# Kernel optimization log

Hardware: AMD Instinct MI355X
Metric: run time of the kernel (lower is better)

The kernel has to match this reference:

```python
import jax, jax.numpy as jnp
import numpy as np

L, D, V, F4 = 12, 768, 50304, 3072
B, T = 4, 1024


def setup_inputs() -> dict:
    key = jax.random.key(0)
    ks = jax.random.split(key, 12)
    s = 0.02
    return {
        "idx": jax.random.randint(ks[0], (B, T), 0, V),
        "targets": jax.random.randint(ks[1], (B, T), 0, V),
        "wte": jax.random.normal(ks[2], (V, D), jnp.float32) * s,  # tied with lm_head
        "pos_embed": jax.random.normal(ks[3], (L, D), jnp.float32),  # per-block (1,1,D) learned pos embed
        "dyt_alpha": jnp.full((L, 3), 0.5, jnp.float32),  # dyt, dyt2, dyt3 alphas
        "dyt_w": jnp.ones((L, 3, D), jnp.float32),
        "dyt_b": jnp.zeros((L, 3, D), jnp.float32),
        "Wq": jax.random.normal(ks[4], (L, D, D), jnp.float32) * s,
        "Wk": jax.random.normal(ks[5], (L, D, D), jnp.float32) * s,
        "Wv": jax.random.normal(ks[6], (L, D, D), jnp.float32) * s,
        "Wp": jax.random.normal(ks[7], (L, D, D), jnp.float32) * s,
        "bp": jnp.zeros((L, D), jnp.float32),
        "We": jax.random.normal(ks[8], (L, F4, D), jnp.float32) * s,
        "be": jnp.zeros((L, F4), jnp.float32),
        "Wc": jax.random.normal(ks[9], (L, D, F4), jnp.float32) * s,
        "bc": jnp.zeros((L, D), jnp.float32),
    }


def _dyt(x, a, w, b):
    return jnp.tanh(a * x) * w + b


def _forward(idx, targets, wte, pos_embed, dyt_alpha, dyt_w, dyt_b,
             Wq, Wk, Wv, Wp, bp, We, be, Wc, bc):
    b, t = idx.shape
    x = wte[idx]  # (b,t,D)
    pos = jnp.arange(t)
    pbias = -jnp.abs(pos[None, :] - pos[:, None]).astype(x.dtype)  # (t,t) ALiBi-style bias
    scale = 1.0 / np.sqrt(D)  # note: source scales by sqrt(emb_dim), not head dim
    total_kl = jnp.asarray(0.0, x.dtype)
    for l in range(L):
        xl = x + pos_embed[l][None, None, :]
        prior = _dyt(xl, dyt_alpha[l, 2], dyt_w[l, 2], dyt_b[l, 2])  # dyt3
        h = _dyt(xl, dyt_alpha[l, 0], dyt_w[l, 0], dyt_b[l, 0])      # dyt (dropout=0)
        Q = jnp.einsum('btd,od->bto', h, Wq[l])
        K = jnp.einsum('btd,od->bto', h, Wk[l])
        Vv = jnp.einsum('btd,od->bto', h, Wv[l])
        scores = jnp.einsum('btd,bsd->bts', Q, K) * scale + pbias  # (b,t,t), no causal mask
        aw = jax.nn.softmax(scores, axis=-1)
        ao = jnp.einsum('bts,bsd->btd', aw, Vv)
        ao = jnp.einsum('btd,od->bto', ao, Wp[l]) + bp[l]
        h2 = _dyt(ao, dyt_alpha[l, 1], dyt_w[l, 1], dyt_b[l, 1])     # dyt2
        h2 = jax.nn.gelu(jnp.einsum('btd,fd->btf', h2, We[l]) + be[l], approximate=False)
        h2 = jnp.einsum('btf,df->btd', h2, Wc[l]) + bc[l]
        posterior = h2 + prior
        m = 0.5 * (prior + posterior)
        lm = jax.nn.log_softmax(m, axis=-1)
        mp = jnp.exp(lm)
        lp = jax.nn.log_softmax(prior, axis=-1)
        lq = jax.nn.log_softmax(posterior, axis=-1)
        # F.kl_div(log_p, q, reduction='batchmean') = sum(q*(log q - log_p)) / batch
        kl = 0.5 * (jnp.sum(mp * (lm - lp)) + jnp.sum(mp * (lm - lq))) / b
        total_kl = total_kl + kl
        x = posterior
    logits = jnp.einsum('btd,vd->btv', x[:, -1:, :], wte)  # (b,1,V)
    full_logits = jnp.einsum('btd,vd->btv', x, wte)
    lsm = jax.nn.log_softmax(full_logits, axis=-1)
    nll = -jnp.take_along_axis(lsm, targets[..., None], axis=-1).squeeze(-1)
    loss = jnp.mean(nll) + total_kl * 0.1
    return logits, loss


def reference(idx, targets, wte, pos_embed, dyt_alpha, dyt_w, dyt_b,
              Wq, Wk, Wv, Wp, bp, We, be, Wc, bc):
    return _forward(idx, targets, wte, pos_embed, dyt_alpha, dyt_w, dyt_b,
                    Wq, Wk, Wv, Wp, bp, We, be, Wc, bc)
```

## Files before the change

kernel.cpp:

```cpp
#include <hip/hip_runtime.h>
#include <hip/hip_bf16.h>

typedef __attribute__((ext_vector_type(8))) short bf16x8;
typedef __attribute__((ext_vector_type(4))) float f32x4;

__device__ __forceinline__ short f2bf(float f) {
  unsigned u = __float_as_uint(f);
  u = u + 0x7fffu + ((u >> 16) & 1u);
  return (short)(u >> 16);
}
__device__ __forceinline__ float bf2f(short s) {
  return __uint_as_float(((unsigned)(unsigned short)s) << 16);
}

#define GLOB_CAST(p) ((const __attribute__((address_space(1))) void*)(p))
#define LDS_CAST(p) ((__attribute__((address_space(3))) void*)(p))
#define GLL16(g, l) __builtin_amdgcn_global_load_lds(GLOB_CAST(g), LDS_CAST(l), 16, 0, 0)

constexpr int EP_BF16 = 0, EP_SCORES = 1, EP_DYT = 2, EP_GELU = 3, EP_PRIOR = 4;

__global__ __launch_bounds__(256) void cvt_k(const float* __restrict__ src,
                                             short* __restrict__ dst, long n4) {
  const long s = (long)blockIdx.x * 256 + threadIdx.x;
  if (s >= n4) return;
  float4 v = ((const float4*)src)[s];
  short4 o = {f2bf(v.x), f2bf(v.y), f2bf(v.z), f2bf(v.w)};
  ((short4*)dst)[s] = o;
}

__global__ __launch_bounds__(256) void cvt_layer_k(
    const float* __restrict__ wq, const float* __restrict__ wk,
    const float* __restrict__ wv, const float* __restrict__ wp,
    const float* __restrict__ we, const float* __restrict__ wc,
    short* __restrict__ dst) {
  const long s = (long)blockIdx.x * 256 + threadIdx.x;
  const long e = s * 4;
  const float* src; long off;
  if (e < 589824)        { src = wq; off = e; }
  else if (e < 1179648)  { src = wk; off = e - 589824; }
  else if (e < 1769472)  { src = wv; off = e - 1179648; }
  else if (e < 2359296)  { src = wp; off = e - 1769472; }
  else if (e < 4718592)  { src = we; off = e - 2359296; }
  else                   { src = wc; off = e - 4718592; }
  float4 v = *(const float4*)(src + off);
  short4 o = {f2bf(v.x), f2bf(v.y), f2bf(v.z), f2bf(v.w)};
  *(short4*)(dst + e) = o;
}

__global__ __launch_bounds__(256) void embed_k(const int* __restrict__ idx,
                                               const float* __restrict__ wte,
                                               float* __restrict__ x) {
  const long s = (long)blockIdx.x * 256 + threadIdx.x;
  const long row = s / 192;
  const int c4 = (int)(s % 192);
  ((float4*)x)[s] = ((const float4*)(wte + (long)idx[row] * 768))[c4];
}

__global__ __launch_bounds__(256) void layerhead_k(
    const float* __restrict__ x, const float* __restrict__ pos,
    const float* __restrict__ alp, const float* __restrict__ w,
    const float* __restrict__ b, float* __restrict__ prior,
    short* __restrict__ h) {
  const long s = (long)blockIdx.x * 256 + threadIdx.x;
  const int c4 = (int)(s % 192);
  float4 xv = ((const float4*)x)[s];
  float4 pv = ((const float4*)pos)[c4];
  float4 w0 = ((const float4*)w)[c4];
  float4 b0 = ((const float4*)b)[c4];
  float4 w2 = ((const float4*)(w + 1536))[c4];
  float4 b2 = ((const float4*)(b + 1536))[c4];
  const float a0 = alp[0], a2 = alp[2];
  float4 xl = {xv.x + pv.x, xv.y + pv.y, xv.z + pv.z, xv.w + pv.w};
  float4 pr = {tanhf(a2 * xl.x) * w2.x + b2.x, tanhf(a2 * xl.y) * w2.y + b2.y,
               tanhf(a2 * xl.z) * w2.z + b2.z, tanhf(a2 * xl.w) * w2.w + b2.w};
  ((float4*)prior)[s] = pr;
  short4 hh = {f2bf(tanhf(a0 * xl.x) * w0.x + b0.x),
               f2bf(tanhf(a0 * xl.y) * w0.y + b0.y),
               f2bf(tanhf(a0 * xl.z) * w0.z + b0.z),
               f2bf(tanhf(a0 * xl.w) * w0.w + b0.w)};
  ((short4*)h)[s] = hh;
}

template <int EP>
__global__ __launch_bounds__(256, 2) void gemm_bt(
    const short* __restrict__ A, const short* __restrict__ B,
    void* __restrict__ Cv, int K, int lda, int ldb, int ldc,
    long sA, long sB, long sC,
    const float* __restrict__ bias, const float* __restrict__ dw,
    const float* __restrict__ db, const float* __restrict__ alp,
    const float* __restrict__ prior, float scale) {
  __shared__ short As[128 * 64];
  __shared__ short Bs[128 * 64];
  const int tid = threadIdx.x, lane = tid & 63;
  const int wr = tid >> 7, wc = (tid >> 6) & 1;
  const long rowBase = (long)blockIdx.y * 128;
  const long colBase = (long)blockIdx.x * 128;
  const short* Ab = A + (long)blockIdx.z * sA;
  const short* Bb = B + (long)blockIdx.z * sB;
  const int srow = tid >> 3, sseg = tid & 7;
  const int ssegS = sseg ^ (srow & 7);

  f32x4 acc[4][4];
#pragma unroll
  for (int m = 0; m < 4; ++m)
#pragma unroll
    for (int n = 0; n < 4; ++n) acc[m][n] = (f32x4){0.f, 0.f, 0.f, 0.f};

  const int q = lane >> 4, cl = lane & 15;
  const int rsw = cl & 7;

  for (int kt = 0; kt < K; kt += 64) {
#pragma unroll
    for (int i = 0; i < 4; ++i) {
      GLL16(Ab + (rowBase + i * 32 + srow) * (long)lda + kt + ssegS * 8,
            As + ((i * 32 + srow) * 64 + sseg * 8));
      GLL16(Bb + (colBase + i * 32 + srow) * (long)ldb + kt + ssegS * 8,
            Bs + ((i * 32 + srow) * 64 + sseg * 8));
    }
    __syncthreads();
#pragma unroll
    for (int kk = 0; kk < 2; ++kk) {
      const int sw = ((kk * 4 + q) ^ rsw) << 3;
      bf16x8 af[4], bfr[4];
#pragma unroll
      for (int m = 0; m < 4; ++m)
        af[m] = *(const bf16x8*)&As[(wr * 64 + m * 16 + cl) * 64 + sw];
#pragma unroll
      for (int n = 0; n < 4; ++n)
        bfr[n] = *(const bf16x8*)&Bs[(wc * 64 + n * 16 + cl) * 64 + sw];
#pragma unroll
      for (int m = 0; m < 4; ++m)
#pragma unroll
        for (int n = 0; n < 4; ++n)
          acc[m][n] = __builtin_amdgcn_mfma_f32_16x16x32_bf16(af[m], bfr[n], acc[m][n], 0, 0, 0);
    }
    __syncthreads();
  }

#pragma unroll
  for (int m = 0; m < 4; ++m) {
#pragma unroll
    for (int n = 0; n < 4; ++n) {
#pragma unroll
      for (int j = 0; j < 4; ++j) {
        long r = rowBase + wr * 64 + m * 16 + q * 4 + j;
        long c = colBase + wc * 64 + n * 16 + cl;
        float v = acc[m][n][j];
        if constexpr (EP == EP_SCORES) {
          float pb = -fabsf((float)(int)(r - c));
          ((float*)Cv)[(long)blockIdx.z * sC + r * ldc + c] = v * scale + pb;
        } else if constexpr (EP == EP_BF16) {
          ((short*)Cv)[(long)blockIdx.z * sC + r * ldc + c] = f2bf(v);
        } else if constexpr (EP == EP_DYT) {
          float xv = v + bias[c];
          ((short*)Cv)[r * (long)ldc + c] = f2bf(tanhf(alp[0] * xv) * dw[c] + db[c]);
        } else if constexpr (EP == EP_GELU) {
          float xv = v + bias[c];
          ((short*)Cv)[r * (long)ldc + c] = f2bf(0.5f * xv * (1.f + erff(xv * 0.70710678118654752f)));
        } else if constexpr (EP == EP_PRIOR) {
          ((float*)Cv)[r * (long)ldc + c] = v + bias[c] + prior[r * (long)ldc + c];
        }
      }
    }
  }
}

__global__ __launch_bounds__(256) void transp_k(const short* __restrict__ V,
                                                short* __restrict__ Vt, int ldv) {
  __shared__ short t[32][33];
  const int b = blockIdx.z;
  const int d0 = blockIdx.x * 32, t0 = blockIdx.y * 32;
  const int tx = threadIdx.x & 31, ty = threadIdx.x >> 5;
  const short* Vb = V + (long)b * 1024 * ldv;
  short* Tb = Vt + (long)b * 768 * 1024;
#pragma unroll
  for (int i = 0; i < 4; ++i)
    t[ty + i * 8][tx] = Vb[(long)(t0 + ty + i * 8) * ldv + d0 + tx];
  __syncthreads();
#pragma unroll
  for (int i = 0; i < 4; ++i)
    Tb[(long)(d0 + ty + i * 8) * 1024 + t0 + tx] = t[tx][ty + i * 8];
}

__global__ __launch_bounds__(256) void softmax_k(const float* __restrict__ sc,
                                                 short* __restrict__ aw) {
  const int lane = threadIdx.x & 63;
  const long row = (long)blockIdx.x * 4 + (threadIdx.x >> 6);
  const float4* p = (const float4*)(sc + row * 1024);
  float4 v[4];
  float mx = -3e38f;
#pragma unroll
  for (int i = 0; i < 4; ++i) {
    v[i] = p[lane * 4 + i];
    mx = fmaxf(mx, fmaxf(fmaxf(v[i].x, v[i].y), fmaxf(v[i].z, v[i].w)));
  }
#pragma unroll
  for (int o = 1; o < 64; o <<= 1) mx = fmaxf(mx, __shfl_xor(mx, o));
  float e[16];
  float s = 0.f;
#pragma unroll
  for (int i = 0; i < 4; ++i) {
    e[i * 4 + 0] = __expf(v[i].x - mx);
    e[i * 4 + 1] = __expf(v[i].y - mx);
    e[i * 4 + 2] = __expf(v[i].z - mx);
    e[i * 4 + 3] = __expf(v[i].w - mx);
    s += e[i * 4] + e[i * 4 + 1] + e[i * 4 + 2] + e[i * 4 + 3];
  }
#pragma unroll
  for (int o = 1; o < 64; o <<= 1) s += __shfl_xor(s, o);
  const float inv = 1.f / s;
  short4* dst = (short4*)(aw + row * 1024);
#pragma unroll
  for (int i = 0; i < 4; ++i) {
    short4 o4 = {f2bf(e[i * 4] * inv), f2bf(e[i * 4 + 1] * inv),
                 f2bf(e[i * 4 + 2] * inv), f2bf(e[i * 4 + 3] * inv)};
    dst[lane * 4 + i] = o4;
  }
}

__global__ __launch_bounds__(256) void kl_k(const float* __restrict__ prior,
                                            const float* __restrict__ post,
                                            double* __restrict__ acc) {
  const int lane = threadIdx.x & 63;
  const long row = (long)blockIdx.x * 4 + (threadIdx.x >> 6);
  const float* pp = prior + row * 768;
  const float* qq = post + row * 768;
  float p[12], q[12];
#pragma unroll
  for (int i = 0; i < 12; ++i) { p[i] = pp[lane + i * 64]; q[i] = qq[lane + i * 64]; }
  float mp = -3e38f, mq = -3e38f, mm = -3e38f;
#pragma unroll
  for (int i = 0; i < 12; ++i) {
    float m = 0.5f * (p[i] + q[i]);
    mp = fmaxf(mp, p[i]); mq = fmaxf(mq, q[i]); mm = fmaxf(mm, m);
  }
#pragma unroll
  for (int o = 1; o < 64; o <<= 1) {
    mp = fmaxf(mp, __shfl_xor(mp, o));
    mq = fmaxf(mq, __shfl_xor(mq, o));
    mm = fmaxf(mm, __shfl_xor(mm, o));
  }
  float sp = 0.f, sq = 0.f, sm = 0.f;
#pragma unroll
  for (int i = 0; i < 12; ++i) {
    sp += __expf(p[i] - mp);
    sq += __expf(q[i] - mq);
    sm += __expf(0.5f * (p[i] + q[i]) - mm);
  }
#pragma unroll
  for (int o = 1; o < 64; o <<= 1) {
    sp += __shfl_xor(sp, o); sq += __shfl_xor(sq, o); sm += __shfl_xor(sm, o);
  }
  const float lseP = mp + logf(sp), lseQ = mq + logf(sq), lseM = mm + logf(sm);
  float kl = 0.f;
#pragma unroll
  for (int i = 0; i < 12; ++i) {
    float m = 0.5f * (p[i] + q[i]);
    float lm = m - lseM;
    kl += __expf(lm) * (2.f * lm - (p[i] - lseP) - (q[i] - lseQ));
  }
#pragma unroll
  for (int o = 1; o < 64; o <<= 1) kl += __shfl_xor(kl, o);
  if (lane == 0) atomicAdd(&acc[0], (double)kl);
}

__global__ __launch_bounds__(256, 2) void lse_gemm_k(
    const short* __restrict__ Xb, const short* __restrict__ Wt,
    float* __restrict__ pm, float* __restrict__ ps,
    float* __restrict__ logits_out, int G) {
  __shared__ short As[128 * 64];
  __shared__ short Bs[128 * 64];
  __shared__ float pmx[2][128], psm[2][128], rm[128], rs[128];
  const int tid = threadIdx.x, lane = tid & 63;
  const int wr = tid >> 7, wc = (tid >> 6) & 1;
  const int g = blockIdx.x;
  const long rowBase = (long)blockIdx.y * 128;
  const int srow = tid >> 3, sseg = tid & 7;
  const int ssegS = sseg ^ (srow & 7);
  const int q = lane >> 4, cl = lane & 15;
  const int rsw = cl & 7;
  if (tid < 128) { rm[tid] = -3e38f; rs[tid] = 0.f; }

  for (int tile = g; tile < 393; tile += G) {
    const long colBase = (long)tile * 128;
    f32x4 acc[4][4];
#pragma unroll
    for (int m = 0; m < 4; ++m)
#pragma unroll
      for (int n = 0; n < 4; ++n) acc[m][n] = (f32x4){0.f, 0.f, 0.f, 0.f};

    for (int kt = 0; kt < 768; kt += 64) {
#pragma unroll
      for (int i = 0; i < 4; ++i) {
        GLL16(Xb + (rowBase + i * 32 + srow) * 768L + kt + ssegS * 8,
              As + ((i * 32 + srow) * 64 + sseg * 8));
        GLL16(Wt + (colBase + i * 32 + srow) * 768L + kt + ssegS * 8,
              Bs + ((i * 32 + srow) * 64 + sseg * 8));
      }
      __syncthreads();
#pragma unroll
      for (int kk = 0; kk < 2; ++kk) {
        const int sw = ((kk * 4 + q) ^ rsw) << 3;
        bf16x8 af[4], bfr[4];
#pragma unroll
        for (int m = 0; m < 4; ++m)
          af[m] = *(const bf16x8*)&As[(wr * 64 + m * 16 + cl) * 64 + sw];
#pragma unroll
        for (int n = 0; n < 4; ++n)
          bfr[n] = *(const bf16x8*)&Bs[(wc * 64 + n * 16 + cl) * 64 + sw];
#pragma unroll
        for (int m = 0; m < 4; ++m)
#pragma unroll
          for (int n = 0; n < 4; ++n)
            acc[m][n] = __builtin_amdgcn_mfma_f32_16x16x32_bf16(af[m], bfr[n], acc[m][n], 0, 0, 0);
      }
      __syncthreads();
    }

#pragma unroll
    for (int m = 0; m < 4; ++m)
#pragma unroll
      for (int n = 0; n < 4; ++n)
#pragma unroll
        for (int j = 0; j < 4; ++j) {
          long r = rowBase + wr * 64 + m * 16 + q * 4 + j;
          if ((r & 1023) == 1023) {
            long c = colBase + wc * 64 + n * 16 + cl;
            logits_out[(r >> 10) * 50304 + c] = acc[m][n][j];
          }
        }

#pragma unroll
    for (int m = 0; m < 4; ++m) {
#pragma unroll
      for (int j = 0; j < 4; ++j) {
        float mx = acc[m][0][j];
#pragma unroll
        for (int n = 1; n < 4; ++n) mx = fmaxf(mx, acc[m][n][j]);
#pragma unroll
        for (int o = 1; o < 16; o <<= 1) mx = fmaxf(mx, __shfl_xor(mx, o));
        float sm = 0.f;
#pragma unroll
        for (int n = 0; n < 4; ++n) sm += __expf(acc[m][n][j] - mx);
#pragma unroll
        for (int o = 1; o < 16; o <<= 1) sm += __shfl_xor(sm, o);
        if (cl == 0) {
          int lr = wr * 64 + m * 16 + q * 4 + j;
          pmx[wc][lr] = mx;
          psm[wc][lr] = sm;
        }
      }
    }
    __syncthreads();
    if (tid < 128) {
      float m0 = pmx[0][tid], m1 = pmx[1][tid];
      float m2 = fmaxf(m0, m1);
      float s2 = psm[0][tid] * __expf(m0 - m2) + psm[1][tid] * __expf(m1 - m2);
      float mo = rm[tid], mn = fmaxf(mo, m2);
      rs[tid] = rs[tid] * __expf(mo - mn) + s2 * __expf(m2 - mn);
      rm[tid] = mn;
    }
    __syncthreads();
  }
  if (tid < 128) {
    long row = rowBase + tid;
    pm[row * G + g] = rm[tid];
    ps[row * G + g] = rs[tid];
  }
}

__global__ __launch_bounds__(256) void tlog_k(const short* __restrict__ xbf,
                                              const short* __restrict__ wtebf,
                                              const int* __restrict__ targets,
                                              float* __restrict__ tlog) {
  const int lane = threadIdx.x & 63;
  const long row = (long)blockIdx.x * 4 + (threadIdx.x >> 6);
  const long tgt = targets[row];
  const short* a = xbf + row * 768;
  const short* b = wtebf + tgt * 768;
  float s = 0.f;
#pragma unroll
  for (int i = 0; i < 12; ++i) s += bf2f(a[lane + i * 64]) * bf2f(b[lane + i * 64]);
#pragma unroll
  for (int o = 1; o < 64; o <<= 1) s += __shfl_xor(s, o);
  if (lane == 0) tlog[row] = s;
}

__global__ __launch_bounds__(256) void stage2_k(const float* __restrict__ pm,
                                                const float* __restrict__ ps,
                                                const float* __restrict__ tlog,
                                                double* __restrict__ acc, int G) {
  const long row = (long)blockIdx.x * 256 + threadIdx.x;
  float M = -3e38f;
  for (int gi = 0; gi < G; ++gi) M = fmaxf(M, pm[row * G + gi]);
  float S = 0.f;
  for (int gi = 0; gi < G; ++gi) S += ps[row * G + gi] * __expf(pm[row * G + gi] - M);
  float nll = (M + logf(S)) - tlog[row];
#pragma unroll
  for (int o = 1; o < 64; o <<= 1) nll += __shfl_xor(nll, o);
  if ((threadIdx.x & 63) == 0) atomicAdd(&acc[1], (double)nll);
}

__global__ void finalize_k(const double* __restrict__ acc, float* __restrict__ out) {
  if (threadIdx.x == 0)
    out[201216] = (float)(acc[1] / 4096.0 + 0.1 * 0.5 * acc[0] / 4.0);
}

constexpr size_t OFF_WTEBF = 0;
constexpr size_t OFF_LW    = 77266944;
constexpr size_t OFF_X     = 91422720;
constexpr size_t OFF_PRIOR = 104005632;
constexpr size_t OFF_H     = 116588544;
constexpr size_t OFF_QKV   = 122880000;
constexpr size_t OFF_VT    = 141754368;
constexpr size_t OFF_SC    = 148045824;
constexpr size_t OFF_AW    = 164823040;
constexpr size_t OFF_AO    = 173211648;
constexpr size_t OFF_H2    = 179503104;
constexpr size_t OFF_E     = 185794560;
constexpr size_t OFF_XBF   = 210960384;
constexpr size_t OFF_PM    = 217251840;
constexpr size_t OFF_PS    = 217645056;
constexpr size_t OFF_TLOG  = 218038272;
constexpr size_t OFF_ACC   = 218054656;
constexpr size_t WS_NEED   = 218055680;

extern "C" void kernel_launch(void* const* d_in, const int* in_sizes, int n_in,
                              void* d_out, int out_size, void* d_ws, size_t ws_size,
                              hipStream_t stream) {
  const int* idx = (const int*)d_in[0];
  const int* targets = (const int*)d_in[1];
  const float* wte = (const float*)d_in[2];
  const float* pos = (const float*)d_in[3];
  const float* dalpha = (const float*)d_in[4];
  const float* dytw = (const float*)d_in[5];
  const float* dytb = (const float*)d_in[6];
  const float* Wq = (const float*)d_in[7];
  const float* Wk = (const float*)d_in[8];
  const float* Wv = (const float*)d_in[9];
  const float* Wp = (const float*)d_in[10];
  const float* bp = (const float*)d_in[11];
  const float* We = (const float*)d_in[12];
  const float* be = (const float*)d_in[13];
  const float* Wc = (const float*)d_in[14];
  const float* bc = (const float*)d_in[15];
  float* out = (float*)d_out;

  if (ws_size < WS_NEED) return;
  char* ws = (char*)d_ws;
  short* WTEBF = (short*)(ws + OFF_WTEBF);
  short* LW = (short*)(ws + OFF_LW);
  float* X = (float*)(ws + OFF_X);
  float* PRIOR = (float*)(ws + OFF_PRIOR);
  short* H = (short*)(ws + OFF_H);
  short* QKVB = (short*)(ws + OFF_QKV);
  short* VT = (short*)(ws + OFF_VT);
  float* SC = (float*)(ws + OFF_SC);
  short* AW = (short*)(ws + OFF_AW);
  short* AO = (short*)(ws + OFF_AO);
  short* H2 = (short*)(ws + OFF_H2);
  short* E = (short*)(ws + OFF_E);
  short* XBF = (short*)(ws + OFF_XBF);
  float* PM = (float*)(ws + OFF_PM);
  float* PS = (float*)(ws + OFF_PS);
  float* TLOG = (float*)(ws + OFF_TLOG);
  double* ACC = (double*)(ws + OFF_ACC);

  hipMemsetAsync(ACC, 0, 16, stream);
  cvt_k<<<37728, 256, 0, stream>>>(wte, WTEBF, 9658368);
  embed_k<<<3072, 256, 0, stream>>>(idx, wte, X);

  const float scale = 0.03608439182435161f;

  for (int l = 0; l < 12; ++l) {
    layerhead_k<<<3072, 256, 0, stream>>>(X, pos + l * 768, dalpha + l * 3,
                                          dytw + l * 2304, dytb + l * 2304, PRIOR, H);
    cvt_layer_k<<<6912, 256, 0, stream>>>(Wq + (long)l * 589824, Wk + (long)l * 589824,
                                          Wv + (long)l * 589824, Wp + (long)l * 589824,
                                          We + (long)l * 2359296, Wc + (long)l * 2359296, LW);
    gemm_bt<EP_BF16><<<dim3(18, 32, 1), 256, 0, stream>>>(
        H, LW, QKVB, 768, 768, 768, 2304, 0, 0, 0,
        nullptr, nullptr, nullptr, nullptr, nullptr, 0.f);
    transp_k<<<dim3(24, 32, 4), 256, 0, stream>>>(QKVB + 1536, VT, 2304);
    gemm_bt<EP_SCORES><<<dim3(8, 8, 4), 256, 0, stream>>>(
        QKVB, QKVB + 768, SC, 768, 2304, 2304, 1024,
        2359296, 2359296, 1048576, nullptr, nullptr, nullptr, nullptr, nullptr, scale);
    softmax_k<<<1024, 256, 0, stream>>>(SC, AW);
    gemm_bt<EP_BF16><<<dim3(6, 8, 4), 256, 0, stream>>>(
        AW, VT, AO, 1024, 1024, 1024, 768, 1048576, 786432, 786432,
        nullptr, nullptr, nullptr, nullptr, nullptr, 0.f);
    gemm_bt<EP_DYT><<<dim3(6, 32, 1), 256, 0, stream>>>(
        AO, LW + 1769472, H2, 768, 768, 768, 768, 0, 0, 0,
        bp + l * 768, dytw + l * 2304 + 768, dytb + l * 2304 + 768,
        dalpha + l * 3 + 1, nullptr, 0.f);
    gemm_bt<EP_GELU><<<dim3(24, 32, 1), 256, 0, stream>>>(
        H2, LW + 2359296, E, 768, 768, 768, 3072, 0, 0, 0,
        be + l * 3072, nullptr, nullptr, nullptr, nullptr, 0.f);
    gemm_bt<EP_PRIOR><<<dim3(6, 32, 1), 256, 0, stream>>>(
        E, LW + 4718592, X, 3072, 3072, 3072, 768, 0, 0, 0,
        bc + l * 768, nullptr, nullptr, nullptr, PRIOR, 0.f);
    kl_k<<<1024, 256, 0, stream>>>(PRIOR, X, ACC);
  }

  cvt_k<<<3072, 256, 0, stream>>>(X, XBF, 786432);
  lse_gemm_k<<<dim3(24, 32), 256, 0, stream>>>(XBF, WTEBF, PM, PS, out, 24);
  tlog_k<<<1024, 256, 0, stream>>>(XBF, WTEBF, targets, TLOG);
  stage2_k<<<16, 256, 0, stream>>>(PM, PS, TLOG, ACC, 24);
  finalize_k<<<1, 64, 0, stream>>>(ACC, out);
}
```

Baseline: 3.387 ms.

## Fuse layer head into KL tail, add narrow GEMM tiles, alias buffers

Merges the embedding with the first layer's DyT head, and folds each next layer's DyT head (or the final bf16 conversion) into the KL kernel, which removes a full-activation read pass and a launch per layer. Softmax now writes bf16 weights in place over the fp32 scores. The GEMM gets a templated N tile width, so the narrow-output GEMMs (scores, AV, proj, FC2) use 64-wide tiles and launch twice as many blocks for better CU occupancy. Workspace buffers are aliased to cut memory footprint, which relies on the stream ordering staying correct.

Measured after the change: 3.111 ms, median of 2. 1.09x faster.

```diff
diff --git a/kernel.cpp b/kernel.cpp
--- a/kernel.cpp
+++ b/kernel.cpp
@@ -47,23 +47,16 @@
   *(short4*)(dst + e) = o;
 }
 
-__global__ __launch_bounds__(256) void embed_k(const int* __restrict__ idx,
-                                               const float* __restrict__ wte,
-                                               float* __restrict__ x) {
+__global__ __launch_bounds__(256) void embed_head_k(
+    const int* __restrict__ idx, const float* __restrict__ wte,
+    const float* __restrict__ pos, const float* __restrict__ alp,
+    const float* __restrict__ w, const float* __restrict__ b,
+    float* __restrict__ x, float* __restrict__ prior, short* __restrict__ h) {
   const long s = (long)blockIdx.x * 256 + threadIdx.x;
   const long row = s / 192;
   const int c4 = (int)(s % 192);
-  ((float4*)x)[s] = ((const float4*)(wte + (long)idx[row] * 768))[c4];
-}
-
-__global__ __launch_bounds__(256) void layerhead_k(
-    const float* __restrict__ x, const float* __restrict__ pos,
-    const float* __restrict__ alp, const float* __restrict__ w,
-    const float* __restrict__ b, float* __restrict__ prior,
-    short* __restrict__ h) {
-  const long s = (long)blockIdx.x * 256 + threadIdx.x;
-  const int c4 = (int)(s % 192);
-  float4 xv = ((const float4*)x)[s];
+  float4 xv = ((const float4*)(wte + (long)idx[row] * 768))[c4];
+  ((float4*)x)[s] = xv;
   float4 pv = ((const float4*)pos)[c4];
   float4 w0 = ((const float4*)w)[c4];
   float4 b0 = ((const float4*)b)[c4];
@@ -81,7 +74,7 @@
   ((short4*)h)[s] = hh;
 }
 
-template <int EP>
+template <int EP, int TN>
 __global__ __launch_bounds__(256, 2) void gemm_bt(
     const short* __restrict__ A, const short* __restrict__ B,
     void* __restrict__ Cv, int K, int lda, int ldb, int ldc,
@@ -89,49 +82,51 @@
     const float* __restrict__ bias, const float* __restrict__ dw,
     const float* __restrict__ db, const float* __restrict__ alp,
     const float* __restrict__ prior, float scale) {
+  constexpr int NF = TN / 32;
   __shared__ short As[128 * 64];
-  __shared__ short Bs[128 * 64];
+  __shared__ short Bs[TN * 64];
   const int tid = threadIdx.x, lane = tid & 63;
   const int wr = tid >> 7, wc = (tid >> 6) & 1;
   const long rowBase = (long)blockIdx.y * 128;
-  const long colBase = (long)blockIdx.x * 128;
+  const long colBase = (long)blockIdx.x * TN;
   const short* Ab = A + (long)blockIdx.z * sA;
   const short* Bb = B + (long)blockIdx.z * sB;
   const int srow = tid >> 3, sseg = tid & 7;
   const int ssegS = sseg ^ (srow & 7);
 
-  f32x4 acc[4][4];
+  f32x4 acc[4][NF];
 #pragma unroll
   for (int m = 0; m < 4; ++m)
 #pragma unroll
-    for (int n = 0; n < 4; ++n) acc[m][n] = (f32x4){0.f, 0.f, 0.f, 0.f};
+    for (int n = 0; n < NF; ++n) acc[m][n] = (f32x4){0.f, 0.f, 0.f, 0.f};
 
   const int q = lane >> 4, cl = lane & 15;
   const int rsw = cl & 7;
 
   for (int kt = 0; kt < K; kt += 64) {
 #pragma unroll
-    for (int i = 0; i < 4; ++i) {
+    for (int i = 0; i < 4; ++i)
       GLL16(Ab + (rowBase + i * 32 + srow) * (long)lda + kt + ssegS * 8,
             As + ((i * 32 + srow) * 64 + sseg * 8));
+#pragma unroll
+    for (int i = 0; i < TN / 32; ++i)
       GLL16(Bb + (colBase + i * 32 + srow) * (long)ldb + kt + ssegS * 8,
             Bs + ((i * 32 + srow) * 64 + sseg * 8));
-    }
     __syncthreads();
 #pragma unroll
     for (int kk = 0; kk < 2; ++kk) {
       const int sw = ((kk * 4 + q) ^ rsw) << 3;
-      bf16x8 af[4], bfr[4];
+      bf16x8 af[4], bfr[NF];
 #pragma unroll
       for (int m = 0; m < 4; ++m)
         af[m] = *(const bf16x8*)&As[(wr * 64 + m * 16 + cl) * 64 + sw];
 #pragma unroll
-      for (int n = 0; n < 4; ++n)
-        bfr[n] = *(const bf16x8*)&Bs[(wc * 64 + n * 16 + cl) * 64 + sw];
+      for (int n = 0; n < NF; ++n)
+        bfr[n] = *(const bf16x8*)&Bs[(wc * (TN / 2) + n * 16 + cl) * 64 + sw];
 #pragma unroll
       for (int m = 0; m < 4; ++m)
 #pragma unroll
-        for (int n = 0; n < 4; ++n)
+        for (int n = 0; n < NF; ++n)
           acc[m][n] = __builtin_amdgcn_mfma_f32_16x16x32_bf16(af[m], bfr[n], acc[m][n], 0, 0, 0);
     }
     __syncthreads();
@@ -140,11 +135,11 @@
 #pragma unroll
   for (int m = 0; m < 4; ++m) {
 #pragma unroll
-    for (int n = 0; n < 4; ++n) {
+    for (int n = 0; n < NF; ++n) {
 #pragma unroll
       for (int j = 0; j < 4; ++j) {
         long r = rowBase + wr * 64 + m * 16 + q * 4 + j;
-        long c = colBase + wc * 64 + n * 16 + cl;
+        long c = colBase + wc * (TN / 2) + n * 16 + cl;
         float v = acc[m][n][j];
         if constexpr (EP == EP_SCORES) {
           float pb = -fabsf((float)(int)(r - c));
@@ -182,8 +177,7 @@
     Tb[(long)(d0 + ty + i * 8) * 1024 + t0 + tx] = t[tx][ty + i * 8];
 }
 
-__global__ __launch_bounds__(256) void softmax_k(const float* __restrict__ sc,
-                                                 short* __restrict__ aw) {
+__global__ __launch_bounds__(256) void softmax_k(float* __restrict__ sc) {
   const int lane = threadIdx.x & 63;
   const long row = (long)blockIdx.x * 4 + (threadIdx.x >> 6);
   const float4* p = (const float4*)(sc + row * 1024);
@@ -209,7 +203,7 @@
 #pragma unroll
   for (int o = 1; o < 64; o <<= 1) s += __shfl_xor(s, o);
   const float inv = 1.f / s;
-  short4* dst = (short4*)(aw + row * 1024);
+  short4* dst = (short4*)((short*)sc + row * 2048);
 #pragma unroll
   for (int i = 0; i < 4; ++i) {
     short4 o4 = {f2bf(e[i * 4] * inv), f2bf(e[i * 4 + 1] * inv),
@@ -218,12 +212,15 @@
   }
 }
 
-__global__ __launch_bounds__(256) void kl_k(const float* __restrict__ prior,
-                                            const float* __restrict__ post,
-                                            double* __restrict__ acc) {
+__global__ __launch_bounds__(256) void tail_k(
+    float* __restrict__ prior, const float* __restrict__ post,
+    const float* __restrict__ pos_n, const float* __restrict__ alp_n,
+    const float* __restrict__ w_n, const float* __restrict__ b_n,
+    short* __restrict__ h, short* __restrict__ xbf,
+    double* __restrict__ acc, int last) {
   const int lane = threadIdx.x & 63;
   const long row = (long)blockIdx.x * 4 + (threadIdx.x >> 6);
-  const float* pp = prior + row * 768;
+  float* pp = prior + row * 768;
   const float* qq = post + row * 768;
   float p[12], q[12];
 #pragma unroll
@@ -262,6 +259,20 @@
 #pragma unroll
   for (int o = 1; o < 64; o <<= 1) kl += __shfl_xor(kl, o);
   if (lane == 0) atomicAdd(&acc[0], (double)kl);
+
+  if (last) {
+#pragma unroll
+    for (int i = 0; i < 12; ++i) xbf[row * 768 + lane + i * 64] = f2bf(q[i]);
+  } else {
+    const float a0 = alp_n[0], a2 = alp_n[2];
+#pragma unroll
+    for (int i = 0; i < 12; ++i) {
+      const int col = lane + i * 64;
+      float xl = q[i] + pos_n[col];
+      pp[col] = tanhf(a2 * xl) * w_n[1536 + col] + b_n[1536 + col];
+      h[row * 768 + col] = f2bf(tanhf(a0 * xl) * w_n[col] + b_n[col]);
+    }
+  }
 }
 
 __global__ __launch_bounds__(256, 2) void lse_gemm_k(
@@ -410,20 +421,19 @@
 constexpr size_t OFF_LW    = 77266944;
 constexpr size_t OFF_X     = 91422720;
 constexpr size_t OFF_PRIOR = 104005632;
-constexpr size_t OFF_H     = 116588544;
-constexpr size_t OFF_QKV   = 122880000;
-constexpr size_t OFF_VT    = 141754368;
+constexpr size_t OFF_HB    = 116588544;
+constexpr size_t OFF_U1    = 122880000;
+constexpr size_t OFF_QKV   = OFF_U1;
+constexpr size_t OFF_VT    = OFF_U1 + 18874368;
+constexpr size_t OFF_E     = OFF_U1;
 constexpr size_t OFF_SC    = 148045824;
-constexpr size_t OFF_AW    = 164823040;
-constexpr size_t OFF_AO    = 173211648;
-constexpr size_t OFF_H2    = 179503104;
-constexpr size_t OFF_E     = 185794560;
-constexpr size_t OFF_XBF   = 210960384;
-constexpr size_t OFF_PM    = 217251840;
-constexpr size_t OFF_PS    = 217645056;
-constexpr size_t OFF_TLOG  = 218038272;
-constexpr size_t OFF_ACC   = 218054656;
-constexpr size_t WS_NEED   = 218055680;
+constexpr size_t OFF_AO    = 164823040;
+constexpr size_t OFF_XBF   = 171114496;
+constexpr size_t OFF_PM    = 177405952;
+constexpr size_t OFF_PS    = 177799168;
+constexpr size_t OFF_TLOG  = 178192384;
+constexpr size_t OFF_ACC   = 178208768;
+constexpr size_t WS_NEED   = 178208784;
 
 extern "C" void kernel_launch(void* const* d_in, const int* in_sizes, int n_in,
                               void* d_out, int out_size, void* d_ws, size_t ws_size,
@@ -452,14 +462,13 @@
   short* LW = (short*)(ws + OFF_LW);
   float* X = (float*)(ws + OFF_X);
   float* PRIOR = (float*)(ws + OFF_PRIOR);
-  short* H = (short*)(ws + OFF_H);
+  short* HB = (short*)(ws + OFF_HB);
   short* QKVB = (short*)(ws + OFF_QKV);
   short* VT = (short*)(ws + OFF_VT);
+  short* E = (short*)(ws + OFF_E);
   float* SC = (float*)(ws + OFF_SC);
-  short* AW = (short*)(ws + OFF_AW);
+  short* AW = (short*)(ws + OFF_SC);
   short* AO = (short*)(ws + OFF_AO);
-  short* H2 = (short*)(ws + OFF_H2);
-  short* E = (short*)(ws + OFF_E);
   short* XBF = (short*)(ws + OFF_XBF);
   float* PM = (float*)(ws + OFF_PM);
   float* PS = (float*)(ws + OFF_PS);
@@ -468,41 +477,40 @@
 
   hipMemsetAsync(ACC, 0, 16, stream);
   cvt_k<<<37728, 256, 0, stream>>>(wte, WTEBF, 9658368);
-  embed_k<<<3072, 256, 0, stream>>>(idx, wte, X);
+  embed_head_k<<<3072, 256, 0, stream>>>(idx, wte, pos, dalpha, dytw, dytb, X, PRIOR, HB);
 
   const float scale = 0.03608439182435161f;
 
   for (int l = 0; l < 12; ++l) {
-    layerhead_k<<<3072, 256, 0, stream>>>(X, pos + l * 768, dalpha + l * 3,
-                                          dytw + l * 2304, dytb + l * 2304, PRIOR, H);
     cvt_layer_k<<<6912, 256, 0, stream>>>(Wq + (long)l * 589824, Wk + (long)l * 589824,
                                           Wv + (long)l * 589824, Wp + (long)l * 589824,
                                           We + (long)l * 2359296, Wc + (long)l * 2359296, LW);
-    gemm_bt<EP_BF16><<<dim3(18, 32, 1), 256, 0, stream>>>(
-        H, LW, QKVB, 768, 768, 768, 2304, 0, 0, 0,
+    gemm_bt<EP_BF16, 128><<<dim3(18, 32, 1), 256, 0, stream>>>(
+        HB, LW, QKVB, 768, 768, 768, 2304, 0, 0, 0,
         nullptr, nullptr, nullptr, nullptr, nullptr, 0.f);
     transp_k<<<dim3(24, 32, 4), 256, 0, stream>>>(QKVB + 1536, VT, 2304);
-    gemm_bt<EP_SCORES><<<dim3(8, 8, 4), 256, 0, stream>>>(
+    gemm_bt<EP_SCORES, 64><<<dim3(16, 8, 4), 256, 0, stream>>>(
         QKVB, QKVB + 768, SC, 768, 2304, 2304, 1024,
         2359296, 2359296, 1048576, nullptr, nullptr, nullptr, nullptr, nullptr, scale);
-    softmax_k<<<1024, 256, 0, stream>>>(SC, AW);
-    gemm_bt<EP_BF16><<<dim3(6, 8, 4), 256, 0, stream>>>(
-        AW, VT, AO, 1024, 1024, 1024, 768, 1048576, 786432, 786432,
+    softmax_k<<<1024, 256, 0, stream>>>(SC);
+    gemm_bt<EP_BF16, 64><<<dim3(12, 8, 4), 256, 0, stream>>>(
+        AW, VT, AO, 1024, 2048, 1024, 768, 2097152, 786432, 786432,
         nullptr, nullptr, nullptr, nullptr, nullptr, 0.f);
-    gemm_bt<EP_DYT><<<dim3(6, 32, 1), 256, 0, stream>>>(
-        AO, LW + 1769472, H2, 768, 768, 768, 768, 0, 0, 0,
+    gemm_bt<EP_DYT, 64><<<dim3(12, 32, 1), 256, 0, stream>>>(
+        AO, LW + 1769472, HB, 768, 768, 768, 768, 0, 0, 0,
         bp + l * 768, dytw + l * 2304 + 768, dytb + l * 2304 + 768,
         dalpha + l * 3 + 1, nullptr, 0.f);
-    gemm_bt<EP_GELU><<<dim3(24, 32, 1), 256, 0, stream>>>(
-        H2, LW + 2359296, E, 768, 768, 768, 3072, 0, 0, 0,
+    gemm_bt<EP_GELU, 128><<<dim3(24, 32, 1), 256, 0, stream>>>(
+        HB, LW + 2359296, E, 768, 768, 768, 3072, 0, 0, 0,
         be + l * 3072, nullptr, nullptr, nullptr, nullptr, 0.f);
-    gemm_bt<EP_PRIOR><<<dim3(6, 32, 1), 256, 0, stream>>>(
+    gemm_bt<EP_PRIOR, 64><<<dim3(12, 32, 1), 256, 0, stream>>>(
         E, LW + 4718592, X, 3072, 3072, 3072, 768, 0, 0, 0,
         bc + l * 768, nullptr, nullptr, nullptr, PRIOR, 0.f);
-    kl_k<<<1024, 256, 0, stream>>>(PRIOR, X, ACC);
-  }
-
-  cvt_k<<<3072, 256, 0, stream>>>(X, XBF, 786432);
+    tail_k<<<1024, 256, 0, stream>>>(PRIOR, X, pos + (l + 1) * 768,
+                                     dalpha + (l + 1) * 3, dytw + (l + 1) * 2304,
+                                     dytb + (l + 1) * 2304, HB, XBF, ACC, l == 11);
+  }
+
   lse_gemm_k<<<dim3(24, 32), 256, 0, stream>>>(XBF, WTEBF, PM, PS, out, 24);
   tlog_k<<<1024, 256, 0, stream>>>(XBF, WTEBF, targets, TLOG);
   stage2_k<<<16, 256, 0, stream>>>(PM, PS, TLOG, ACC, 24);
```
